# Kernel tuning notes

Measured on AMD Instinct MI355X. Metric: run time of the kernel, lower is better.

The kernel has to match this reference:

```python
import jax, jax.numpy as jnp
import numpy as np
from jax import lax

B, V, T, D = 64, 32, 50, 16
H_LSTM = 256
GAT_UNITS, N_HEADS = 256, 4


def _lstm(x, Wx, Wh, b):
    # x: [N, T, D] -> [N, T, H]; Keras gate order i, f, g(c), o
    N = x.shape[0]
    Hd = Wh.shape[0]
    xz = jnp.einsum('ntd,dk->ntk', x, Wx) + b  # precompute input projections [N,T,4H]

    def step(carry, z_t):
        h, c = carry
        z = z_t + h @ Wh
        i, f, g, o = jnp.split(z, 4, axis=-1)
        i = jax.nn.sigmoid(i)
        f = jax.nn.sigmoid(f)
        g = jnp.tanh(g)
        o = jax.nn.sigmoid(o)
        c = f * c + i * g
        h = o * jnp.tanh(c)
        return (h, c), h

    init = (jnp.zeros((N, Hd), x.dtype), jnp.zeros((N, Hd), x.dtype))
    _, hs = lax.scan(step, init, jnp.swapaxes(xz, 0, 1))  # [T,N,H]
    return jnp.swapaxes(hs, 0, 1)


def _gat(x, W, a_src, a_dst, bias, src, dst):
    # x: [B, V, F]; star-graph GAT, multi-head, concat heads, gelu activation
    Bb, Vv, _ = x.shape
    units = W.shape[1]
    dh = units // N_HEADS
    h = (x @ W).reshape(Bb, Vv, N_HEADS, dh)             # [B,V,H,dh]
    es = jnp.einsum('bvhd,hd->bvh', h, a_src)            # source attention logits
    ed = jnp.einsum('bvhd,hd->bvh', h, a_dst)            # target attention logits
    e = jax.nn.leaky_relu(es[:, src] + ed[:, dst], 0.2)  # [B,E,H]
    seg_max = jax.vmap(lambda s: jax.ops.segment_max(s, dst, num_segments=Vv))(e)
    ex = jnp.exp(e - lax.stop_gradient(seg_max[:, dst]))
    denom = jax.vmap(lambda s: jax.ops.segment_sum(s, dst, num_segments=Vv))(ex)
    alpha = ex / (denom[:, dst] + 1e-9)                  # segment softmax over incoming edges
    msg = alpha[..., None] * h[:, src]                   # [B,E,H,dh]
    out = jax.vmap(lambda m: jax.ops.segment_sum(m, dst, num_segments=Vv))(msg)
    return jax.nn.gelu(out.reshape(Bb, Vv, units) + bias)


def setup_inputs() -> dict:
    key = jax.random.key(0)
    ks = jax.random.split(key, 16)
    s = lambda k, *sh: jax.random.normal(k, sh, dtype=jnp.float32) * 0.05
    inp = {
        'states': jax.random.normal(ks[0], (B, V, T, D), dtype=jnp.float32),
        # LSTM layer 1
        'Wx1': s(ks[1], D, 4 * H_LSTM), 'Wh1': s(ks[2], H_LSTM, 4 * H_LSTM), 'b1': jnp.zeros((4 * H_LSTM,), jnp.float32),
        # LSTM layer 2
        'Wx2': s(ks[3], H_LSTM, 4 * H_LSTM), 'Wh2': s(ks[4], H_LSTM, 4 * H_LSTM), 'b2': jnp.zeros((4 * H_LSTM,), jnp.float32),
        # GAT layer 1
        'gW1': s(ks[5], H_LSTM, GAT_UNITS), 'ga_src1': s(ks[6], N_HEADS, GAT_UNITS // N_HEADS),
        'ga_dst1': s(ks[7], N_HEADS, GAT_UNITS // N_HEADS), 'gb1': jnp.zeros((GAT_UNITS,), jnp.float32),
        # GAT layer 2
        'gW2': s(ks[8], GAT_UNITS, GAT_UNITS), 'ga_src2': s(ks[9], N_HEADS, GAT_UNITS // N_HEADS),
        'ga_dst2': s(ks[10], N_HEADS, GAT_UNITS // N_HEADS), 'gb2': jnp.zeros((GAT_UNITS,), jnp.float32),
    }
    # undirected star graph: edges u->0 and 0->u (matches __init__: u+v, v+u)
    u = np.arange(V, dtype=np.int32)
    v = np.zeros(V, dtype=np.int32)
    inp['src'] = jnp.asarray(np.concatenate([u, v]))
    inp['dst'] = jnp.asarray(np.concatenate([v, u]))
    return inp


def reference(states, Wx1, Wh1, b1, Wx2, Wh2, b2,
              gW1, ga_src1, ga_dst1, gb1, gW2, ga_src2, ga_dst2, gb2, src, dst):
    x = states.reshape(B * V, T, D)
    x = _lstm(x, Wx1, Wh1, b1)
    x = _lstm(x, Wx2, Wh2, b2)
    x = jnp.mean(x, axis=1)            # GlobalAveragePooling1D over time
    x = x.reshape(B, V, H_LSTM)
    x = _gat(x, gW1, ga_src1, ga_dst1, gb1, src, dst)
    x = _gat(x, gW2, ga_src2, ga_dst2, gb2, src, dst)
    return x  # [B, V, GAT_UNITS]
```

## Files before the change

### kernel.cpp

```cpp
#include <hip/hip_runtime.h>

#define TSTEPS 50
#define NB (2048 * 256)

typedef __attribute__((ext_vector_type(8))) short short8;
typedef __attribute__((ext_vector_type(4))) float f32x4;

__device__ __forceinline__ float sigm(float x) { return 1.0f / (1.0f + expf(-x)); }
__device__ __forceinline__ float gelu_t(float x) {
  float x3 = x * x * x;
  return 0.5f * x * (1.0f + tanhf(0.7978845608028654f * (x + 0.044715f * x3)));
}

__device__ __forceinline__ f32x4 mfma_bf16(short8 a, short8 b, f32x4 c) {
  return __builtin_amdgcn_mfma_f32_16x16x32_bf16(a, b, c, 0, 0, 0);
}

__device__ __forceinline__ ushort f2bf(float x) {
  unsigned u = __builtin_bit_cast(unsigned, x);
  return (ushort)((u + 0x7FFFu + ((u >> 16) & 1u)) >> 16);
}
__device__ __forceinline__ float bf2f(ushort b) {
  unsigned u = (unsigned)b << 16;
  return __builtin_bit_cast(float, u);
}
__device__ __forceinline__ void bsplit(float x, ushort& hi, ushort& lo) {
  hi = f2bf(x);
  lo = f2bf(x - bf2f(hi));
}

__device__ __forceinline__ void mg_barrier(unsigned* bar, unsigned target) {
  __syncthreads();
  if (threadIdx.x == 0) {
    __threadfence();
    atomicAdd(bar, 1u);
    while (atomicAdd(bar, 0u) < target) __builtin_amdgcn_s_sleep(4);
    __threadfence();
  }
  __syncthreads();
}

__global__ void __launch_bounds__(256)
prep(const float* __restrict__ states,
     const float* __restrict__ Wx1, const float* __restrict__ Wh1,
     const float* __restrict__ Wx2, const float* __restrict__ Wh2,
     ushort* __restrict__ xh, ushort* __restrict__ xl,
     ushort* __restrict__ wm1, ushort* __restrict__ wm2,
     unsigned* __restrict__ bar)
{
  const size_t idx = (size_t)blockIdx.x * 256 + threadIdx.x;
  if (blockIdx.x == 0 && threadIdx.x < 256) bar[threadIdx.x] = 0u;
  if (idx < 1638400) {
    ushort h, l; bsplit(states[idx], h, l);
    xh[idx] = h; xl[idx] = l;
  }
  if (idx < 589824) {
    int e = (int)idx;
    int i = e & 7, lane = (e >> 3) & 63, pl = (e >> 9) & 1;
    int s = (e >> 10) % 18, jg = e / 18432;
    int ks = s % 9, nt = s / 9;
    int col = (nt * 2 + ((lane >> 3) & 1)) * 256 + jg * 8 + (lane & 7);
    int kg = ks * 32 + ((lane >> 4) & 3) * 8 + i;
    float w = 0.0f;
    if (ks == 0) { if (kg < 16) w = Wx1[kg * 1024 + col]; }
    else w = Wh1[(kg - 32) * 1024 + col];
    ushort h, l; bsplit(w, h, l);
    wm1[e] = pl ? l : h;
  }
  if (idx < 1048576) {
    int e = (int)idx;
    int i = e & 7, lane = (e >> 3) & 63, pl = (e >> 9) & 1;
    int s = (e >> 10) & 31, jg = e >> 15;
    int ks = s & 15, nt = s >> 4;
    int col = (nt * 2 + ((lane >> 3) & 1)) * 256 + jg * 8 + (lane & 7);
    int kg = ks * 32 + ((lane >> 4) & 3) * 8 + i;
    float w = (kg < 256) ? Wx2[kg * 1024 + col] : Wh2[(kg - 256) * 1024 + col];
    ushort h, l; bsplit(w, h, l);
    wm2[e] = pl ? l : h;
  }
}

__global__ void __launch_bounds__(1024, 1)
lstm_fused(const ushort* __restrict__ xh, const ushort* __restrict__ xl,
           const ushort* __restrict__ wm1, const ushort* __restrict__ wm2,
           const float* __restrict__ b1, const float* __restrict__ b2,
           ushort* __restrict__ hp, float* __restrict__ xg,
           unsigned* __restrict__ bar)
{
  __shared__ __align__(16) ushort W1s[18432];
  __shared__ __align__(16) ushort W2s[32768];

  const int tid = threadIdx.x;
  const int lane = tid & 63;
  const int w = __builtin_amdgcn_readfirstlane(tid >> 6);
  const int lw = w >> 3, mt2 = w & 7;
  const int blk = blockIdx.x;
  const int mg = blk & 7, jg = blk >> 3;
  const int mgbase = mg << 8;
  const int gA = (lane >> 3) & 1;
  const int jcolg = (jg << 3) + (lane & 7);
  unsigned* mybar = bar + (mg << 4);

  {
    const uint4* s1 = (const uint4*)(wm1 + (size_t)jg * 18432);
    uint4* d1 = (uint4*)W1s;
    for (int i = tid; i < 2304; i += 1024) d1[i] = s1[i];
    const uint4* s2 = (const uint4*)(wm2 + (size_t)jg * 32768);
    uint4* d2 = (uint4*)W2s;
    for (int i = tid; i < 4096; i += 1024) d2[i] = s2[i];
  }
  __syncthreads();

  const float* bl = lw ? b2 : b1;
  const float bn0 = bl[gA * 256 + jcolg];
  const float bn1 = bl[(2 + gA) * 256 + jcolg];
  const f32x4 bv0 = {bn0, bn0, bn0, bn0};
  const f32x4 bv1 = {bn1, bn1, bn1, bn1};

  float cst[2][4] = {{0,0,0,0},{0,0,0,0}};
  float pool[2][4] = {{0,0,0,0},{0,0,0,0}};
  f32x4 acc[2][2];

  const int rowb0 = mt2 * 16 + (lane & 15);
  const int rowb1 = rowb0 + 128;
  const int kq = lane >> 4;
  const char* w1c = (const char*)W1s;
  const char* w2c = (const char*)W2s;
  const size_t arow0 = (size_t)(mgbase + rowb0) * 512;
  const size_t arow1 = (size_t)(mgbase + rowb1) * 512;

  auto tri = [&](f32x4 c, short8 ah, short8 al, short8 bh, short8 blo) {
    c = mfma_bf16(ah, bh, c);
    c = mfma_bf16(ah, blo, c);
    c = mfma_bf16(al, bh, c);
    return c;
  };

  for (int p = 0; p <= TSTEPS; ++p) {
    const bool doL1 = (p < TSTEPS), doL2 = (p >= 1), doH2 = (p >= 2);
    const ushort* rdh = hp + (size_t)(((p + 1) & 1) * 2) * 1048576;
    const ushort* rdl = rdh + 1048576;
    ushort* wrh = hp + (size_t)((p & 1) * 2) * 1048576;
    ushort* wrl = wrh + 1048576;
    const bool meL1 = (lw == 0) && doL1;
    const bool meL2 = (lw == 1) && doL2;

    if (meL1 || meL2) { acc[0][0] = bv0; acc[0][1] = bv1; acc[1][0] = bv0; acc[1][1] = bv1; }

    if (meL1) {
      short8 Ah0 = {0,0,0,0,0,0,0,0}, Al0 = {0,0,0,0,0,0,0,0};
      short8 Ah1 = {0,0,0,0,0,0,0,0}, Al1 = {0,0,0,0,0,0,0,0};
      if (kq < 2) {
        const size_t xo0 = (size_t)(mgbase + rowb0) * 800 + p * 16 + kq * 8;
        const size_t xo1 = (size_t)(mgbase + rowb1) * 800 + p * 16 + kq * 8;
        Ah0 = *(const short8*)(xh + xo0);
        Al0 = *(const short8*)(xl + xo0);
        Ah1 = *(const short8*)(xh + xo1);
        Al1 = *(const short8*)(xl + xo1);
      }
      {
        const short8 B00 = *(const short8*)(w1c + (0 * 2 + 0) * 1024 + lane * 16);
        const short8 B01 = *(const short8*)(w1c + (0 * 2 + 1) * 1024 + lane * 16);
        const short8 B10 = *(const short8*)(w1c + (18 + 0) * 1024 + lane * 16);
        const short8 B11 = *(const short8*)(w1c + (18 + 1) * 1024 + lane * 16);
        acc[0][0] = tri(acc[0][0], Ah0, Al0, B00, B01);
        acc[0][1] = tri(acc[0][1], Ah0, Al0, B10, B11);
        acc[1][0] = tri(acc[1][0], Ah1, Al1, B00, B01);
        acc[1][1] = tri(acc[1][1], Ah1, Al1, B10, B11);
      }
      if (p >= 1) {
        #pragma unroll 4
        for (int ks = 1; ks <= 8; ++ks) {
          const size_t ko = (size_t)((ks - 1) * 32 + kq * 8);
          const short8 Ah0h = *(const short8*)(rdh + arow0 + ko);
          const short8 Al0h = *(const short8*)(rdl + arow0 + ko);
          const short8 Ah1h = *(const short8*)(rdh + arow1 + ko);
          const short8 Al1h = *(const short8*)(rdl + arow1 + ko);
          const short8 B00 = *(const short8*)(w1c + ((0 * 9 + ks) * 2 + 0) * 1024 + lane * 16);
          const short8 B01 = *(const short8*)(w1c + ((0 * 9 + ks) * 2 + 1) * 1024 + lane * 16);
          const short8 B10 = *(const short8*)(w1c + ((1 * 9 + ks) * 2 + 0) * 1024 + lane * 16);
          const short8 B11 = *(const short8*)(w1c + ((1 * 9 + ks) * 2 + 1) * 1024 + lane * 16);
          acc[0][0] = tri(acc[0][0], Ah0h, Al0h, B00, B01);
          acc[0][1] = tri(acc[0][1], Ah0h, Al0h, B10, B11);
          acc[1][0] = tri(acc[1][0], Ah1h, Al1h, B00, B01);
          acc[1][1] = tri(acc[1][1], Ah1h, Al1h, B10, B11);
        }
      }
    }
    if (meL2) {
      const int ksend = doH2 ? 16 : 8;
      #pragma unroll 4
      for (int ks = 0; ks < ksend; ++ks) {
        const size_t ko = (size_t)(ks * 32 + kq * 8);
        const short8 Ah0h = *(const short8*)(rdh + arow0 + ko);
        const short8 Al0h = *(const short8*)(rdl + arow0 + ko);
        const short8 Ah1h = *(const short8*)(rdh + arow1 + ko);
        const short8 Al1h = *(const short8*)(rdl + arow1 + ko);
        const short8 B00 = *(const short8*)(w2c + ((0 * 16 + ks) * 2 + 0) * 1024 + lane * 16);
        const short8 B01 = *(const short8*)(w2c + ((0 * 16 + ks) * 2 + 1) * 1024 + lane * 16);
        const short8 B10 = *(const short8*)(w2c + ((1 * 16 + ks) * 2 + 0) * 1024 + lane * 16);
        const short8 B11 = *(const short8*)(w2c + ((1 * 16 + ks) * 2 + 1) * 1024 + lane * 16);
        acc[0][0] = tri(acc[0][0], Ah0h, Al0h, B00, B01);
        acc[0][1] = tri(acc[0][1], Ah0h, Al0h, B10, B11);
        acc[1][0] = tri(acc[1][0], Ah1h, Al1h, B00, B01);
        acc[1][1] = tri(acc[1][1], Ah1h, Al1h, B10, B11);
      }
    }

    if (meL1 || meL2) {
      #pragma unroll
      for (int mtl = 0; mtl < 2; ++mtl) {
        #pragma unroll
        for (int r = 0; r < 4; ++r) {
          const float zA = acc[mtl][0][r];
          const float zB = acc[mtl][1][r];
          const float pA = __shfl_xor(zA, 8);
          const float pB = __shfl_xor(zB, 8);
          const float iv = sigm(zA), fv = sigm(pA);
          const float gv = tanhf(zB), ov = sigm(pB);
          const float cc = fv * cst[mtl][r] + iv * gv;
          cst[mtl][r] = cc;
          const float h = ov * tanhf(cc);
          if (gA == 0) {
            const int seq = mgbase + (mt2 + 8 * mtl) * 16 + (lane >> 4) * 4 + r;
            ushort hu, lu; bsplit(h, hu, lu);
            const size_t base = (size_t)seq * 512 + lw * 256 + jcolg;
            wrh[base] = hu; wrl[base] = lu;
            if (lw) pool[mtl][r] += h;
          }
        }
      }
    }

    if (p < TSTEPS) mg_barrier(mybar, (unsigned)(p + 1) * 32u);
  }

  if (lw == 1 && gA == 0) {
    #pragma unroll
    for (int mtl = 0; mtl < 2; ++mtl)
      #pragma unroll
      for (int r = 0; r < 4; ++r) {
        const int seq = mgbase + (mt2 + 8 * mtl) * 16 + (lane >> 4) * 4 + r;
        xg[(size_t)seq * 256 + jcolg] = pool[mtl][r] * (1.0f / 50.0f);
      }
  }
}

__global__ void __launch_bounds__(256)
gat_feat(const float* __restrict__ xin, const float* __restrict__ gW,
         const float* __restrict__ a_src, const float* __restrict__ a_dst,
         float* __restrict__ hfeat, float* __restrict__ es, float* __restrict__ ed)
{
  __shared__ float Xs[8][260];
  const int tid = threadIdx.x;
  const int r0 = blockIdx.x << 3;
  #pragma unroll
  for (int i = 0; i < 8; ++i) Xs[i][tid] = xin[((r0 + i) << 8) + tid];
  __syncthreads();
  float acc[8];
  #pragma unroll
  for (int i = 0; i < 8; ++i) acc[i] = 0.0f;
  for (int k = 0; k < 256; k += 4) {
    const float w0 = gW[(k + 0) * 256 + tid];
    const float w1 = gW[(k + 1) * 256 + tid];
    const float w2 = gW[(k + 2) * 256 + tid];
    const float w3 = gW[(k + 3) * 256 + tid];
    #pragma unroll
    for (int i = 0; i < 8; ++i)
      acc[i] += Xs[i][k] * w0 + Xs[i][k + 1] * w1 + Xs[i][k + 2] * w2 + Xs[i][k + 3] * w3;
  }
  const int h = tid >> 6;
  const int lane = tid & 63;
  const float asv = a_src[(h << 6) + lane];
  const float adv = a_dst[(h << 6) + lane];
  #pragma unroll
  for (int i = 0; i < 8; ++i) {
    hfeat[((r0 + i) << 8) + tid] = acc[i];
    float pse = acc[i] * asv;
    float pde = acc[i] * adv;
    #pragma unroll
    for (int off = 32; off > 0; off >>= 1) {
      pse += __shfl_down(pse, off);
      pde += __shfl_down(pde, off);
    }
    if (lane == 0) {
      es[((r0 + i) << 2) + h] = pse;
      ed[((r0 + i) << 2) + h] = pde;
    }
  }
}

__global__ void __launch_bounds__(256)
gat_out(const float* __restrict__ hfeat, const float* __restrict__ es, const float* __restrict__ ed,
        const float* __restrict__ gb, float* __restrict__ yout)
{
  __shared__ float exs[32][4];
  __shared__ float invden[4];
  const int tid = threadIdx.x;
  const int rbase = blockIdx.x << 5;
  if (tid < 128) {
    const int u = tid >> 2, h = tid & 3;
    float l = es[((rbase + u) << 2) + h] + ed[(rbase << 2) + h];
    exs[u][h] = (l < 0.0f) ? 0.2f * l : l;
  }
  __syncthreads();
  if (tid < 4) {
    const int h = tid;
    float m = -1e30f;
    for (int u = 0; u < 32; ++u) m = fmaxf(m, exs[u][h]);
    float s = 0.0f;
    for (int u = 0; u < 32; ++u) { float e = expf(exs[u][h] - m); exs[u][h] = e; s += e; }
    s += exs[0][h];
    invden[h] = 1.0f / (s + 1e-9f);
  }
  __syncthreads();
  const int h = tid >> 6;
  const float h0 = hfeat[(rbase << 8) + tid];
  float s = exs[0][h] * h0;
  for (int u = 0; u < 32; ++u)
    s += exs[u][h] * hfeat[((rbase + u) << 8) + tid];
  const float bias = gb[tid];
  const float inv1 = 1.0f / (1.0f + 1e-9f);
  yout[(rbase << 8) + tid] = gelu_t(s * invden[h] + bias);
  const float gv = gelu_t(h0 * inv1 + bias);
  for (int v = 1; v < 32; ++v)
    yout[((rbase + v) << 8) + tid] = gv;
}

extern "C" void kernel_launch(void* const* d_in, const int* in_sizes, int n_in,
                              void* d_out, int out_size, void* d_ws, size_t ws_size,
                              hipStream_t stream) {
  (void)in_sizes; (void)n_in; (void)out_size; (void)ws_size;
  const float* states = (const float*)d_in[0];
  const float* Wx1 = (const float*)d_in[1];
  const float* Wh1 = (const float*)d_in[2];
  const float* b1  = (const float*)d_in[3];
  const float* Wx2 = (const float*)d_in[4];
  const float* Wh2 = (const float*)d_in[5];
  const float* b2  = (const float*)d_in[6];
  const float* gW1 = (const float*)d_in[7];
  const float* gas1 = (const float*)d_in[8];
  const float* gad1 = (const float*)d_in[9];
  const float* gb1 = (const float*)d_in[10];
  const float* gW2 = (const float*)d_in[11];
  const float* gas2 = (const float*)d_in[12];
  const float* gad2 = (const float*)d_in[13];
  const float* gb2 = (const float*)d_in[14];

  char* wsb = (char*)d_ws;
  ushort* hp  = (ushort*)wsb;
  ushort* xh  = (ushort*)(wsb + 8388608);
  ushort* xl  = xh + 1638400;
  ushort* wm1 = (ushort*)(wsb + 8388608 + 6553600);
  ushort* wm2 = wm1 + 589824;
  float*  xg  = (float*)(wsb + 8388608 + 6553600 + 1179648 + 2097152);
  unsigned* bar = (unsigned*)((char*)xg + 2097152);
  float* y1    = (float*)wsb;
  float* hfeat = y1 + NB;
  float* es    = hfeat + NB;
  float* ed    = es + 2048 * 4;
  float* dout  = (float*)d_out;

  prep<<<dim3(6400), dim3(256), 0, stream>>>(states, Wx1, Wh1, Wx2, Wh2,
                                             xh, xl, wm1, wm2, bar);

  void* args[] = { (void*)&xh, (void*)&xl, (void*)&wm1, (void*)&wm2,
                   (void*)&b1, (void*)&b2, (void*)&hp, (void*)&xg, (void*)&bar };
  hipError_t err = hipLaunchCooperativeKernel((void*)lstm_fused, dim3(256), dim3(1024),
                                              args, 0, stream);
  if (err != hipSuccess) {
    lstm_fused<<<dim3(256), dim3(1024), 0, stream>>>(xh, xl, wm1, wm2,
                                                     b1, b2, hp, xg, bar);
  }

  gat_feat<<<dim3(256), dim3(256), 0, stream>>>(xg, gW1, gas1, gad1, hfeat, es, ed);
  gat_out<<<dim3(64), dim3(256), 0, stream>>>(hfeat, es, ed, gb1, y1);
  gat_feat<<<dim3(256), dim3(256), 0, stream>>>(y1, gW2, gas2, gad2, hfeat, es, ed);
  gat_out<<<dim3(64), dim3(256), 0, stream>>>(hfeat, es, ed, gb2, dout);
}
```

Baseline: 1.933 ms.

## Have each wave compute both LSTM layers for one m-tile, sharing h1 loads

The persistent LSTM kernel previously gave half the waves layer 1 and half layer 2, each covering two 16-row tiles. Now every wave covers one 16-row tile and computes both layers. The h1 fragments it loads once from global memory feed both the layer-1 recurrent product and the layer-2 input product, which removes duplicate loads of the same rows and balances work across all waves. In exchange, each wave runs both layers' gate math back to back, and register pressure per wave shifts.

```diff
diff --git a/kernel.cpp b/kernel.cpp
--- a/kernel.cpp
+++ b/kernel.cpp
@@ -92,8 +92,7 @@
 
   const int tid = threadIdx.x;
   const int lane = tid & 63;
-  const int w = __builtin_amdgcn_readfirstlane(tid >> 6);
-  const int lw = w >> 3, mt2 = w & 7;
+  const int mt = __builtin_amdgcn_readfirstlane(tid >> 6);
   const int blk = blockIdx.x;
   const int mg = blk & 7, jg = blk >> 3;
   const int mgbase = mg << 8;
@@ -111,23 +110,23 @@
   }
   __syncthreads();
 
-  const float* bl = lw ? b2 : b1;
-  const float bn0 = bl[gA * 256 + jcolg];
-  const float bn1 = bl[(2 + gA) * 256 + jcolg];
-  const f32x4 bv0 = {bn0, bn0, bn0, bn0};
-  const f32x4 bv1 = {bn1, bn1, bn1, bn1};
-
-  float cst[2][4] = {{0,0,0,0},{0,0,0,0}};
-  float pool[2][4] = {{0,0,0,0},{0,0,0,0}};
-  f32x4 acc[2][2];
-
-  const int rowb0 = mt2 * 16 + (lane & 15);
-  const int rowb1 = rowb0 + 128;
+  const float b1n0 = b1[gA * 256 + jcolg];
+  const float b1n1 = b1[(2 + gA) * 256 + jcolg];
+  const float b2n0 = b2[gA * 256 + jcolg];
+  const float b2n1 = b2[(2 + gA) * 256 + jcolg];
+  const f32x4 bv10 = {b1n0, b1n0, b1n0, b1n0};
+  const f32x4 bv11 = {b1n1, b1n1, b1n1, b1n1};
+  const f32x4 bv20 = {b2n0, b2n0, b2n0, b2n0};
+  const f32x4 bv21 = {b2n1, b2n1, b2n1, b2n1};
+
+  float c1s[4] = {0,0,0,0}, c2s[4] = {0,0,0,0}, pool[4] = {0,0,0,0};
+  f32x4 a1[2], a2[2];
+
+  const int rowb = mt * 16 + (lane & 15);
   const int kq = lane >> 4;
   const char* w1c = (const char*)W1s;
   const char* w2c = (const char*)W2s;
-  const size_t arow0 = (size_t)(mgbase + rowb0) * 512;
-  const size_t arow1 = (size_t)(mgbase + rowb1) * 512;
+  const size_t arow = (size_t)(mgbase + rowb) * 512;
 
   auto tri = [&](f32x4 c, short8 ah, short8 al, short8 bh, short8 blo) {
     c = mfma_bf16(ah, bh, c);
@@ -142,107 +141,108 @@
     const ushort* rdl = rdh + 1048576;
     ushort* wrh = hp + (size_t)((p & 1) * 2) * 1048576;
     ushort* wrl = wrh + 1048576;
-    const bool meL1 = (lw == 0) && doL1;
-    const bool meL2 = (lw == 1) && doL2;
-
-    if (meL1 || meL2) { acc[0][0] = bv0; acc[0][1] = bv1; acc[1][0] = bv0; acc[1][1] = bv1; }
-
-    if (meL1) {
-      short8 Ah0 = {0,0,0,0,0,0,0,0}, Al0 = {0,0,0,0,0,0,0,0};
-      short8 Ah1 = {0,0,0,0,0,0,0,0}, Al1 = {0,0,0,0,0,0,0,0};
+
+    if (doL1) { a1[0] = bv10; a1[1] = bv11; }
+    if (doL2) { a2[0] = bv20; a2[1] = bv21; }
+
+    if (doL1) {
+      short8 Ah = {0,0,0,0,0,0,0,0}, Al = {0,0,0,0,0,0,0,0};
       if (kq < 2) {
-        const size_t xo0 = (size_t)(mgbase + rowb0) * 800 + p * 16 + kq * 8;
-        const size_t xo1 = (size_t)(mgbase + rowb1) * 800 + p * 16 + kq * 8;
-        Ah0 = *(const short8*)(xh + xo0);
-        Al0 = *(const short8*)(xl + xo0);
-        Ah1 = *(const short8*)(xh + xo1);
-        Al1 = *(const short8*)(xl + xo1);
-      }
-      {
-        const short8 B00 = *(const short8*)(w1c + (0 * 2 + 0) * 1024 + lane * 16);
-        const short8 B01 = *(const short8*)(w1c + (0 * 2 + 1) * 1024 + lane * 16);
-        const short8 B10 = *(const short8*)(w1c + (18 + 0) * 1024 + lane * 16);
-        const short8 B11 = *(const short8*)(w1c + (18 + 1) * 1024 + lane * 16);
-        acc[0][0] = tri(acc[0][0], Ah0, Al0, B00, B01);
-        acc[0][1] = tri(acc[0][1], Ah0, Al0, B10, B11);
-        acc[1][0] = tri(acc[1][0], Ah1, Al1, B00, B01);
-        acc[1][1] = tri(acc[1][1], Ah1, Al1, B10, B11);
-      }
-      if (p >= 1) {
-        #pragma unroll 4
-        for (int ks = 1; ks <= 8; ++ks) {
-          const size_t ko = (size_t)((ks - 1) * 32 + kq * 8);
-          const short8 Ah0h = *(const short8*)(rdh + arow0 + ko);
-          const short8 Al0h = *(const short8*)(rdl + arow0 + ko);
-          const short8 Ah1h = *(const short8*)(rdh + arow1 + ko);
-          const short8 Al1h = *(const short8*)(rdl + arow1 + ko);
-          const short8 B00 = *(const short8*)(w1c + ((0 * 9 + ks) * 2 + 0) * 1024 + lane * 16);
-          const short8 B01 = *(const short8*)(w1c + ((0 * 9 + ks) * 2 + 1) * 1024 + lane * 16);
-          const short8 B10 = *(const short8*)(w1c + ((1 * 9 + ks) * 2 + 0) * 1024 + lane * 16);
-          const short8 B11 = *(const short8*)(w1c + ((1 * 9 + ks) * 2 + 1) * 1024 + lane * 16);
-          acc[0][0] = tri(acc[0][0], Ah0h, Al0h, B00, B01);
-          acc[0][1] = tri(acc[0][1], Ah0h, Al0h, B10, B11);
-          acc[1][0] = tri(acc[1][0], Ah1h, Al1h, B00, B01);
-          acc[1][1] = tri(acc[1][1], Ah1h, Al1h, B10, B11);
+        const size_t xo = (size_t)(mgbase + rowb) * 800 + p * 16 + kq * 8;
+        Ah = *(const short8*)(xh + xo);
+        Al = *(const short8*)(xl + xo);
+      }
+      const short8 B00 = *(const short8*)(w1c + 0 * 1024 + lane * 16);
+      const short8 B01 = *(const short8*)(w1c + 1 * 1024 + lane * 16);
+      const short8 B10 = *(const short8*)(w1c + 18 * 1024 + lane * 16);
+      const short8 B11 = *(const short8*)(w1c + 19 * 1024 + lane * 16);
+      a1[0] = tri(a1[0], Ah, Al, B00, B01);
+      a1[1] = tri(a1[1], Ah, Al, B10, B11);
+    }
+    if (doL2) {
+      #pragma unroll
+      for (int ks = 0; ks < 8; ++ks) {
+        const size_t ko = (size_t)(ks * 32 + kq * 8);
+        const short8 Ah = *(const short8*)(rdh + arow + ko);
+        const short8 Al = *(const short8*)(rdl + arow + ko);
+        if (doL1) {
+          const short8 B00 = *(const short8*)(w1c + ((0 * 9 + ks + 1) * 2 + 0) * 1024 + lane * 16);
+          const short8 B01 = *(const short8*)(w1c + ((0 * 9 + ks + 1) * 2 + 1) * 1024 + lane * 16);
+          const short8 B10 = *(const short8*)(w1c + ((1 * 9 + ks + 1) * 2 + 0) * 1024 + lane * 16);
+          const short8 B11 = *(const short8*)(w1c + ((1 * 9 + ks + 1) * 2 + 1) * 1024 + lane * 16);
+          a1[0] = tri(a1[0], Ah, Al, B00, B01);
+          a1[1] = tri(a1[1], Ah, Al, B10, B11);
         }
-      }
-    }
-    if (meL2) {
-      const int ksend = doH2 ? 16 : 8;
-      #pragma unroll 4
-      for (int ks = 0; ks < ksend; ++ks) {
-        const size_t ko = (size_t)(ks * 32 + kq * 8);
-        const short8 Ah0h = *(const short8*)(rdh + arow0 + ko);
-        const short8 Al0h = *(const short8*)(rdl + arow0 + ko);
-        const short8 Ah1h = *(const short8*)(rdh + arow1 + ko);
-        const short8 Al1h = *(const short8*)(rdl + arow1 + ko);
-        const short8 B00 = *(const short8*)(w2c + ((0 * 16 + ks) * 2 + 0) * 1024 + lane * 16);
-        const short8 B01 = *(const short8*)(w2c + ((0 * 16 + ks) * 2 + 1) * 1024 + lane * 16);
-        const short8 B10 = *(const short8*)(w2c + ((1 * 16 + ks) * 2 + 0) * 1024 + lane * 16);
-        const short8 B11 = *(const short8*)(w2c + ((1 * 16 + ks) * 2 + 1) * 1024 + lane * 16);
-        acc[0][0] = tri(acc[0][0], Ah0h, Al0h, B00, B01);
-        acc[0][1] = tri(acc[0][1], Ah0h, Al0h, B10, B11);
-        acc[1][0] = tri(acc[1][0], Ah1h, Al1h, B00, B01);
-        acc[1][1] = tri(acc[1][1], Ah1h, Al1h, B10, B11);
-      }
-    }
-
-    if (meL1 || meL2) {
-      #pragma unroll
-      for (int mtl = 0; mtl < 2; ++mtl) {
+        const short8 C00 = *(const short8*)(w2c + ((0 * 16 + ks) * 2 + 0) * 1024 + lane * 16);
+        const short8 C01 = *(const short8*)(w2c + ((0 * 16 + ks) * 2 + 1) * 1024 + lane * 16);
+        const short8 C10 = *(const short8*)(w2c + ((1 * 16 + ks) * 2 + 0) * 1024 + lane * 16);
+        const short8 C11 = *(const short8*)(w2c + ((1 * 16 + ks) * 2 + 1) * 1024 + lane * 16);
+        a2[0] = tri(a2[0], Ah, Al, C00, C01);
+        a2[1] = tri(a2[1], Ah, Al, C10, C11);
+      }
+      if (doH2) {
         #pragma unroll
-        for (int r = 0; r < 4; ++r) {
-          const float zA = acc[mtl][0][r];
-          const float zB = acc[mtl][1][r];
-          const float pA = __shfl_xor(zA, 8);
-          const float pB = __shfl_xor(zB, 8);
-          const float iv = sigm(zA), fv = sigm(pA);
-          const float gv = tanhf(zB), ov = sigm(pB);
-          const float cc = fv * cst[mtl][r] + iv * gv;
-          cst[mtl][r] = cc;
-          const float h = ov * tanhf(cc);
-          if (gA == 0) {
-            const int seq = mgbase + (mt2 + 8 * mtl) * 16 + (lane >> 4) * 4 + r;
-            ushort hu, lu; bsplit(h, hu, lu);
-            const size_t base = (size_t)seq * 512 + lw * 256 + jcolg;
-            wrh[base] = hu; wrl[base] = lu;
-            if (lw) pool[mtl][r] += h;
-          }
+        for (int ks = 8; ks < 16; ++ks) {
+          const size_t ko = (size_t)(ks * 32 + kq * 8);
+          const short8 Ah = *(const short8*)(rdh + arow + ko);
+          const short8 Al = *(const short8*)(rdl + arow + ko);
+          const short8 C00 = *(const short8*)(w2c + ((0 * 16 + ks) * 2 + 0) * 1024 + lane * 16);
+          const short8 C01 = *(const short8*)(w2c + ((0 * 16 + ks) * 2 + 1) * 1024 + lane * 16);
+          const short8 C10 = *(const short8*)(w2c + ((1 * 16 + ks) * 2 + 0) * 1024 + lane * 16);
+          const short8 C11 = *(const short8*)(w2c + ((1 * 16 + ks) * 2 + 1) * 1024 + lane * 16);
+          a2[0] = tri(a2[0], Ah, Al, C00, C01);
+          a2[1] = tri(a2[1], Ah, Al, C10, C11);
         }
       }
     }
 
-    if (p < TSTEPS) mg_barrier(mybar, (unsigned)(p + 1) * 32u);
-  }
-
-  if (lw == 1 && gA == 0) {
-    #pragma unroll
-    for (int mtl = 0; mtl < 2; ++mtl)
+    if (doL1) {
       #pragma unroll
       for (int r = 0; r < 4; ++r) {
-        const int seq = mgbase + (mt2 + 8 * mtl) * 16 + (lane >> 4) * 4 + r;
-        xg[(size_t)seq * 256 + jcolg] = pool[mtl][r] * (1.0f / 50.0f);
-      }
+        const float zA = a1[0][r], zB = a1[1][r];
+        const float pA = __shfl_xor(zA, 8), pB = __shfl_xor(zB, 8);
+        const float iv = sigm(zA), fv = sigm(pA);
+        const float gv = tanhf(zB), ov = sigm(pB);
+        const float cc = fv * c1s[r] + iv * gv;
+        c1s[r] = cc;
+        const float h = ov * tanhf(cc);
+        if (gA == 0) {
+          const int seq = mgbase + mt * 16 + (lane >> 4) * 4 + r;
+          ushort hu, lu; bsplit(h, hu, lu);
+          const size_t base = (size_t)seq * 512 + jcolg;
+          wrh[base] = hu; wrl[base] = lu;
+        }
+      }
+    }
+    if (doL2) {
+      #pragma unroll
+      for (int r = 0; r < 4; ++r) {
+        const float zA = a2[0][r], zB = a2[1][r];
+        const float pA = __shfl_xor(zA, 8), pB = __shfl_xor(zB, 8);
+        const float iv = sigm(zA), fv = sigm(pA);
+        const float gv = tanhf(zB), ov = sigm(pB);
+        const float cc = fv * c2s[r] + iv * gv;
+        c2s[r] = cc;
+        const float h = ov * tanhf(cc);
+        pool[r] += h;
+        if (gA == 0) {
+          const int seq = mgbase + mt * 16 + (lane >> 4) * 4 + r;
+          ushort hu, lu; bsplit(h, hu, lu);
+          const size_t base = (size_t)seq * 512 + 256 + jcolg;
+          wrh[base] = hu; wrl[base] = lu;
+        }
+      }
+    }
+
+    if (p < TSTEPS) mg_barrier(mybar, (unsigned)(p + 1) * 32u);
+  }
+
+  if (gA == 0) {
+    #pragma unroll
+    for (int r = 0; r < 4; ++r) {
+      const int seq = mgbase + mt * 16 + (lane >> 4) * 4 + r;
+      xg[(size_t)seq * 256 + jcolg] = pool[r] * (1.0f / 50.0f);
+    }
   }
 }
 
```

New measurement: 1.669 ms. 13.7% less time.
